# Optimization experiments

Measured on AMD Instinct MI355X. Metric: run time of the kernel, lower is better.

## Reference

```python
import jax, jax.numpy as jnp
import numpy as np
import math

N_HEADS = 16
D_HEAD = 128
D_ROPE = 32
SPLIT = D_HEAD - D_ROPE  # 96
LATENT = 512
D_MODEL = 2048
B, T = 2, 2048


def _rotary_emb(num_tokens, d_rope):
    inv_freq = 1.0 / (10000.0 ** (jnp.arange(0, d_rope, 2, dtype=jnp.float32) / d_rope))
    t = jnp.arange(num_tokens, dtype=jnp.float32)
    freqs = jnp.einsum('t,f->tf', t, inv_freq)          # [T, d_rope/2]
    return jnp.concatenate([freqs, freqs], axis=-1)      # [T, d_rope]


def _apply_rotary(x, cos, sin):
    # x: [B,T,H,d_rope]; cos/sin: [1,T,1,d_rope]
    half = x.shape[-1] // 2
    x1, x2 = x[..., :half], x[..., half:]
    rot = jnp.concatenate([-x2, x1], axis=-1)
    return x * cos + rot * sin


def setup_inputs() -> dict:
    key = jax.random.key(0)
    ks = jax.random.split(key, 20)
    s = 0.02
    def w(k, i, o):
        return jax.random.normal(k, (i, o), dtype=jnp.float32) * s
    inp = {
        'input': jax.random.normal(ks[0], (B, T, D_MODEL), dtype=jnp.float32),
        'batch_size': B,
        'num_tokens': T,
        'Wdkv_w': w(ks[1], D_MODEL, LATENT), 'Wdkv_b': jnp.zeros((LATENT,), jnp.float32),
        'Wdq_w':  w(ks[2], D_MODEL, LATENT), 'Wdq_b':  jnp.zeros((LATENT,), jnp.float32),
        'Wuk_w':  w(ks[3], LATENT, N_HEADS * SPLIT),  'Wuk_b': jnp.zeros((N_HEADS * SPLIT,), jnp.float32),
        'Wuv_w':  w(ks[4], LATENT, N_HEADS * D_HEAD), 'Wuv_b': jnp.zeros((N_HEADS * D_HEAD,), jnp.float32),
        'Wuq_w':  w(ks[5], LATENT, N_HEADS * SPLIT),  'Wuq_b': jnp.zeros((N_HEADS * SPLIT,), jnp.float32),
        'Wqr_w':  w(ks[6], LATENT, N_HEADS * D_ROPE), 'Wqr_b': jnp.zeros((N_HEADS * D_ROPE,), jnp.float32),
        'Wkr_w':  w(ks[7], D_MODEL, N_HEADS * D_ROPE), 'Wkr_b': jnp.zeros((N_HEADS * D_ROPE,), jnp.float32),
        'Wo_w':   w(ks[8], N_HEADS * D_HEAD, D_MODEL), 'Wo_b': jnp.zeros((D_MODEL,), jnp.float32),
    }
    return inp


def reference(input, batch_size, num_tokens,
              Wdkv_w, Wdkv_b, Wdq_w, Wdq_b, Wuk_w, Wuk_b, Wuv_w, Wuv_b,
              Wuq_w, Wuq_b, Wqr_w, Wqr_b, Wkr_w, Wkr_b, Wo_w, Wo_b):
    lin = lambda x, w, b: x @ w + b
    bsz, T_ = batch_size, num_tokens

    c_kv = lin(input, Wdkv_w, Wdkv_b)                                   # [B,T,latent]
    k_base = lin(c_kv, Wuk_w, Wuk_b).reshape(bsz, T_, N_HEADS, SPLIT)
    v = lin(c_kv, Wuv_w, Wuv_b).reshape(bsz, T_, N_HEADS, D_HEAD)

    c_q = lin(input, Wdq_w, Wdq_b)
    q_base = lin(c_q, Wuq_w, Wuq_b).reshape(bsz, T_, N_HEADS, SPLIT)
    q_rot = lin(c_q, Wqr_w, Wqr_b).reshape(bsz, T_, N_HEADS, D_ROPE)

    emb = _rotary_emb(T_, D_ROPE)                                        # [T,d_rope]
    cos = jnp.cos(emb)[None, :, None, :]
    sin = jnp.sin(emb)[None, :, None, :]
    q_rot = _apply_rotary(q_rot, cos, sin)
    k_rot = _apply_rotary(lin(input, Wkr_w, Wkr_b).reshape(bsz, T_, N_HEADS, D_ROPE), cos, sin)

    q = jnp.concatenate([q_base, q_rot], axis=-1)                        # [B,T,H,d_head]
    k = jnp.concatenate([k_base, k_rot], axis=-1)

    scores = jnp.einsum('bqhd,bkhd->bhqk', q, k) / math.sqrt(D_HEAD)
    attn = jax.nn.softmax(scores, axis=-1)
    out = jnp.einsum('bhqk,bkhd->bqhd', attn, v)
    out = lin(out.reshape(bsz, T_, N_HEADS * D_HEAD), Wo_w, Wo_b)
    return out, c_kv, k_rot
```

## Files before the change

kernel.cpp:

```cpp
#include <hip/hip_runtime.h>

typedef __bf16 bf16x8 __attribute__((ext_vector_type(8)));
typedef float f32x4 __attribute__((ext_vector_type(4)));
typedef float f32x16 __attribute__((ext_vector_type(16)));

#define NROWS 4096
#define DM 2048
#define LAT 512
#define NH 16
#define DH 128

__device__ __forceinline__ unsigned short f2bf(float f) {
    union { float f; unsigned u; } v; v.f = f;
    unsigned r = v.u + 0x7fffu + ((v.u >> 16) & 1u);
    return (unsigned short)(r >> 16);
}
__device__ __forceinline__ void gload16(const void* g, void* l) {
    __builtin_amdgcn_global_load_lds((const __attribute__((address_space(1))) unsigned int*)g,
                                     (__attribute__((address_space(3))) unsigned int*)l, 16, 0, 0);
}
__device__ __forceinline__ unsigned cvtpk_bf16(float lo, float hi) {
    unsigned r;
    asm("v_cvt_pk_bf16_f32 %0, %1, %2" : "=v"(r) : "v"(lo), "v"(hi));
    return r;
}
__device__ __forceinline__ void pl32swap(unsigned& a, unsigned& b) {
    asm("v_permlane32_swap_b32 %0, %1" : "+v"(a), "+v"(b));
}
__device__ __forceinline__ float exp2a(float x) {
    float r;
    asm("v_exp_f32 %0, %1" : "=v"(r) : "v"(x));
    return r;
}

struct PrepParams {
    const float* tsrc[8]; unsigned short* tdst[8];
    int tK[8]; int tN[8]; int tstart[8];
    const float* input; unsigned short* xbf;
    float* cs; float* sn;
    const float* bsrc[8]; float* bdst[8]; int blen[8];
};

#define PREP_T_END   9984
#define PREP_X_END   18176
#define PREP_R_END   18304
#define PREP_B_END   18340

__global__ __launch_bounds__(256) void prep_kernel(PrepParams P) {
    const int bid = blockIdx.x, tid = threadIdx.x;
    if (bid < PREP_T_END) {
        int j = 0;
        #pragma unroll
        for (int i = 1; i < 8; ++i) if (bid >= P.tstart[i]) j = i;
        const int local = bid - P.tstart[j];
        const float* W = P.tsrc[j];
        unsigned short* Wt = P.tdst[j];
        const int K = P.tK[j], N = P.tN[j];
        const int nbx = N >> 5;
        const int nb = (local % nbx) * 32, kb = (local / nbx) * 32;
        __shared__ float tile[32][33];
        const int tx = tid & 31, ty = tid >> 5;
        #pragma unroll
        for (int i = 0; i < 32; i += 8)
            tile[ty + i][tx] = W[(size_t)(kb + ty + i) * N + nb + tx];
        __syncthreads();
        #pragma unroll
        for (int i = 0; i < 32; i += 8)
            Wt[(size_t)(nb + ty + i) * K + kb + tx] = f2bf(tile[tx][ty + i]);
    } else if (bid < PREP_X_END) {
        const int i = ((bid - PREP_T_END) * 256 + tid) * 4;
        float4 v = *(const float4*)(P.input + i);
        unsigned short* y = P.xbf + i;
        y[0] = f2bf(v.x); y[1] = f2bf(v.y); y[2] = f2bf(v.z); y[3] = f2bf(v.w);
    } else if (bid < PREP_R_END) {
        const int idx = (bid - PREP_X_END) * 256 + tid;
        const int i = idx & 15, t = idx >> 4;
        float inv = powf(10000.0f, -(float)i / 16.0f);
        float a = (float)t * inv;
        P.cs[idx] = cosf(a);
        P.sn[idx] = sinf(a);
    } else {
        const int gid = (bid - PREP_R_END) * 256 + tid;
        int off = 0;
        #pragma unroll
        for (int i = 0; i < 8; ++i) {
            if (gid >= off && gid < off + P.blen[i])
                P.bdst[i][gid - off] = P.bsrc[i][gid - off];
            off += P.blen[i];
        }
    }
}

__global__ __launch_bounds__(256) void gemm_fused_kernel(const unsigned short* __restrict__ A,
                                                         const unsigned short* __restrict__ Bt,
                                                         const float* __restrict__ biascat,
                                                         int K, int which,
                                                         float* __restrict__ outF,
                                                         unsigned short* __restrict__ outB0,
                                                         unsigned short* __restrict__ outB1,
                                                         unsigned short* __restrict__ outB0k,
                                                         float* __restrict__ outRope,
                                                         const float* __restrict__ cs,
                                                         const float* __restrict__ sn) {
    __shared__ __align__(16) unsigned short SM[2][8192];
    const int tid = threadIdx.x;
    const int mb = blockIdx.x * 128;
    const int by = blockIdx.y, nb = by * 128;
    const int w = tid >> 6, lane = tid & 63;
    const int wr = (w >> 1) * 64, wc = (w & 1) * 64;
    const int l15 = lane & 15, l4 = lane >> 4;
    const int srow = lane >> 2, sko = (lane & 3) * 8;

    f32x4 acc[4][4] = {};

    auto STAGE = [&](int buf, int k0) {
        #pragma unroll
        for (int c = 0; c < 16; c += 4) {
            int cc = c + w;
            if (cc < 8)
                gload16(A + (size_t)(mb + cc * 16 + srow) * K + k0 + sko, SM[buf] + cc * 512);
            else
                gload16(Bt + (size_t)(nb + (cc - 8) * 16 + srow) * K + k0 + sko, SM[buf] + 4096 + (cc - 8) * 512);
        }
    };

    const int nk = K >> 5;
    STAGE(0, 0);
    for (int kt = 0; kt < nk; ++kt) {
        const int buf = kt & 1;
        if (kt + 1 < nk) {
            STAGE(buf ^ 1, (kt + 1) << 5);
            asm volatile("s_waitcnt vmcnt(4)" ::: "memory");
        } else {
            asm volatile("s_waitcnt vmcnt(0)" ::: "memory");
        }
        __builtin_amdgcn_sched_barrier(0);
        __builtin_amdgcn_s_barrier();
        __builtin_amdgcn_sched_barrier(0);

        const unsigned short* As = SM[buf];
        const unsigned short* Bs = SM[buf] + 4096;
        bf16x8 af[4], bfr[4];
        #pragma unroll
        for (int mi = 0; mi < 4; ++mi)
            af[mi] = *(const bf16x8*)(As + (wr + mi * 16 + l15) * 32 + l4 * 8);
        #pragma unroll
        for (int ni = 0; ni < 4; ++ni)
            bfr[ni] = *(const bf16x8*)(Bs + (wc + ni * 16 + l15) * 32 + l4 * 8);
        #pragma unroll
        for (int mi = 0; mi < 4; ++mi)
            #pragma unroll
            for (int ni = 0; ni < 4; ++ni)
                acc[mi][ni] = __builtin_amdgcn_mfma_f32_16x16x32_bf16(af[mi], bfr[ni], acc[mi][ni], 0, 0, 0);
        __builtin_amdgcn_s_barrier();
    }

    if (which == 1 && by >= 12) {
        unsigned short* BT = &SM[0][0];
        const int c2b = nb - 1536;
        #pragma unroll
        for (int half = 0; half < 2; ++half) {
            __syncthreads();
            if ((wr >> 6) == half) {
                #pragma unroll
                for (int mi = 0; mi < 4; ++mi)
                    #pragma unroll
                    for (int ni = 0; ni < 4; ++ni) {
                        const int col = wc + ni * 16 + l15;
                        const float bv = biascat[nb + col];
                        ushort4 pv;
                        pv.x = f2bf(acc[mi][ni][0] + bv);
                        pv.y = f2bf(acc[mi][ni][1] + bv);
                        pv.z = f2bf(acc[mi][ni][2] + bv);
                        pv.w = f2bf(acc[mi][ni][3] + bv);
                        *(ushort4*)(BT + col * 72 + mi * 16 + l4 * 4) = pv;
                    }
            }
            __syncthreads();
            const int c = tid >> 1;
            #pragma unroll
            for (int j = 0; j < 4; ++j) {
                const int seg = (tid & 1) * 4 + j;
                uint4 val = *(const uint4*)(BT + c * 72 + seg * 8);
                *(uint4*)(outB1 + (size_t)(c2b + c) * 4096 + mb + half * 64 + seg * 8) = val;
            }
        }
        return;
    }

    #pragma unroll
    for (int mi = 0; mi < 4; ++mi) {
        const int row0 = mb + wr + mi * 16 + l4 * 4;
        #pragma unroll
        for (int ni = 0; ni < 4; ++ni) {
            const int colg = nb + wc + ni * 16 + l15;
            const float bv = biascat[colg];
            float v[4];
            #pragma unroll
            for (int r = 0; r < 4; ++r) v[r] = acc[mi][ni][r] + bv;

            if (which == 0) {
                if (by < 4) {
                    #pragma unroll
                    for (int r = 0; r < 4; ++r) {
                        outF[(size_t)(row0 + r) * 512 + colg] = v[r];
                        outB0[(size_t)(row0 + r) * 512 + colg] = f2bf(v[r]);
                    }
                } else if (by < 8) {
                    const int c2 = colg - 512;
                    #pragma unroll
                    for (int r = 0; r < 4; ++r)
                        outB1[(size_t)(row0 + r) * 512 + c2] = f2bf(v[r]);
                } else {
                    const int cloc = colg - 1024, i2 = cloc & 31, h2 = cloc >> 5;
                    const float pbv = biascat[colg ^ 16];
                    const bool lo = (ni & 1) == 0;
                    #pragma unroll
                    for (int r = 0; r < 4; ++r) {
                        float vp = acc[mi][ni ^ 1][r] + pbv;
                        int t = (row0 + r) & 2047;
                        float cc_ = cs[t * 16 + (i2 & 15)], ss_ = sn[t * 16 + (i2 & 15)];
                        float o = lo ? (v[r] * cc_ - vp * ss_) : (v[r] * cc_ + vp * ss_);
                        outRope[(size_t)(row0 + r) * 512 + cloc] = o;
                        outB0k[(size_t)(row0 + r) * 2048 + h2 * 128 + 96 + i2] = f2bf(o);
                    }
                }
            } else if (which == 1) {
                const int ocol = (colg / 96) * 128 + colg % 96;
                #pragma unroll
                for (int r = 0; r < 4; ++r)
                    outB0[(size_t)(row0 + r) * 2048 + ocol] = f2bf(v[r]);
            } else if (which == 2) {
                if (by < 12) {
                    const int ocol = (colg / 96) * 128 + colg % 96;
                    #pragma unroll
                    for (int r = 0; r < 4; ++r)
                        outB0[(size_t)(row0 + r) * 2048 + ocol] = f2bf(v[r]);
                } else {
                    const int cloc = colg - 1536, i2 = cloc & 31, h2 = cloc >> 5;
                    const float pbv = biascat[colg ^ 16];
                    const bool lo = (ni & 1) == 0;
                    #pragma unroll
                    for (int r = 0; r < 4; ++r) {
                        float vp = acc[mi][ni ^ 1][r] + pbv;
                        int t = (row0 + r) & 2047;
                        float cc_ = cs[t * 16 + (i2 & 15)], ss_ = sn[t * 16 + (i2 & 15)];
                        float o = lo ? (v[r] * cc_ - vp * ss_) : (v[r] * cc_ + vp * ss_);
                        outB0[(size_t)(row0 + r) * 2048 + h2 * 128 + 96 + i2] = f2bf(o);
                    }
                }
            } else {
                #pragma unroll
                for (int r = 0; r < 4; ++r)
                    outF[(size_t)(row0 + r) * 2048 + colg] = v[r];
            }
        }
    }
}

__global__ __launch_bounds__(256, 2) void attn_kernel(const unsigned short* __restrict__ Q,
                                                      const unsigned short* __restrict__ Kb,
                                                      const unsigned short* __restrict__ Vtg,
                                                      unsigned short* __restrict__ O) {
    __shared__ __align__(16) unsigned short Ks[2][64 * 128];
    __shared__ __align__(16) unsigned short Vs[2][128 * 64];

    const int tid = threadIdx.x, w = tid >> 6, lane = tid & 63;
    const int l31 = lane & 31, hi = lane >> 5;
    const int bid = blockIdx.x;
    const int logical = (bid & 7) * 64 + (bid >> 3);
    const int bh = logical >> 4, b = bh >> 4, h = bh & 15;
    const int qt = (logical & 15) * 128 + w * 32;
    const int qrow = qt + l31;
    const float sl2e = 0.08838834764831845f * 1.4426950408889634f;

    bf16x8 qf[8];
    const unsigned short* qptr = Q + (size_t)(b * 2048 + qrow) * 2048 + h * 128 + hi * 8;
    #pragma unroll
    for (int s = 0; s < 8; ++s) qf[s] = *(const bf16x8*)(qptr + s * 16);

    f32x16 acc[4] = {};
    float m_run = -1e30f, l_run = 0.0f;

    const int kl15 = lane >> 4, kd0 = lane & 15;
    const int vr = lane >> 3, vk = lane & 7;

    auto STAGE = [&](int buf, int kt) {
        #pragma unroll
        for (int i = 0; i < 4; ++i) {
            int c = w * 4 + i;
            int key = c * 4 + kl15;
            int d0 = (kd0 * 8) ^ ((key & 7) << 3);
            gload16(Kb + (size_t)(b * 2048 + kt + key) * 2048 + h * 128 + d0, &Ks[buf][c * 512]);
            int dv = c * 8 + vr;
            int k0 = (vk * 8) ^ ((dv & 7) << 3);
            gload16(Vtg + (size_t)(h * 128 + dv) * 4096 + b * 2048 + kt + k0, &Vs[buf][c * 512]);
        }
    };

    STAGE(0, 0);

    for (int t = 0; t < 32; ++t) {
        const int buf = t & 1;
        if (t < 31) {
            STAGE(buf ^ 1, (t + 1) * 64);
            asm volatile("s_waitcnt vmcnt(8)" ::: "memory");
        } else {
            asm volatile("s_waitcnt vmcnt(0)" ::: "memory");
        }
        __builtin_amdgcn_sched_barrier(0);
        __builtin_amdgcn_s_barrier();
        __builtin_amdgcn_sched_barrier(0);

        #pragma unroll
        for (int g = 0; g < 2; ++g) {
            const int key = g * 32 + l31;
            const unsigned short* kbase = &Ks[buf][key * 128];
            const int ksw = (key & 7) << 3;
            f32x16 sc = {};
            __builtin_amdgcn_s_setprio(1);
            #pragma unroll
            for (int s = 0; s < 8; ++s) {
                bf16x8 kf = *(const bf16x8*)(kbase + ((s * 16 + hi * 8) ^ ksw));
                sc = __builtin_amdgcn_mfma_f32_32x32x16_bf16(kf, qf[s], sc, 0, 0, 0);
            }
            __builtin_amdgcn_s_setprio(0);

            float pm = sc[0];
            #pragma unroll
            for (int i = 1; i < 16; ++i) pm = fmaxf(pm, sc[i]);
            pm = fmaxf(pm, __shfl_xor(pm, 32, 64));

            if (__any(pm > m_run + 90.51f)) {
                float mn = fmaxf(m_run, pm);
                float f = exp2a((m_run - mn) * sl2e);
                m_run = mn;
                l_run *= f;
                #pragma unroll
                for (int dg = 0; dg < 4; ++dg)
                    #pragma unroll
                    for (int i = 0; i < 16; ++i) acc[dg][i] *= f;
            }
            const float mexp2 = m_run * sl2e;

            float rs = 0.0f;
            #pragma unroll
            for (int s2 = 0; s2 < 2; ++s2) {
                float e[8];
                #pragma unroll
                for (int j = 0; j < 8; ++j) {
                    e[j] = exp2a(fmaf(sc[s2 * 8 + j], sl2e, -mexp2));
                    rs += e[j];
                }
                unsigned X0 = cvtpk_bf16(e[0], e[1]), X1 = cvtpk_bf16(e[2], e[3]);
                unsigned Y0 = cvtpk_bf16(e[4], e[5]), Y1 = cvtpk_bf16(e[6], e[7]);
                pl32swap(X0, Y0);
                pl32swap(X1, Y1);
                union { unsigned u[4]; bf16x8 v; } pf;
                pf.u[0] = X0; pf.u[1] = X1; pf.u[2] = Y0; pf.u[3] = Y1;

                const int kofs = g * 32 + s2 * 16 + hi * 8;
                __builtin_amdgcn_s_setprio(1);
                #pragma unroll
                for (int dg = 0; dg < 4; ++dg) {
                    const int d = dg * 32 + l31;
                    bf16x8 vf = *(const bf16x8*)(&Vs[buf][d * 64 + (kofs ^ ((d & 7) << 3))]);
                    acc[dg] = __builtin_amdgcn_mfma_f32_32x32x16_bf16(vf, pf.v, acc[dg], 0, 0, 0);
                }
                __builtin_amdgcn_s_setprio(0);
            }
            rs += __shfl_xor(rs, 32, 64);
            l_run += rs;
        }
        __builtin_amdgcn_s_barrier();
    }

    const float inv = 1.0f / l_run;
    unsigned short* obase = O + (size_t)(b * 2048 + qrow) * 2048 + h * 128;
    #pragma unroll
    for (int dg = 0; dg < 4; ++dg)
        #pragma unroll
        for (int k = 0; k < 4; ++k) {
            ushort4 pv;
            pv.x = f2bf(acc[dg][4 * k + 0] * inv);
            pv.y = f2bf(acc[dg][4 * k + 1] * inv);
            pv.z = f2bf(acc[dg][4 * k + 2] * inv);
            pv.w = f2bf(acc[dg][4 * k + 3] * inv);
            *(ushort4*)(obase + dg * 32 + k * 8 + hi * 4) = pv;
        }
}

extern "C" void kernel_launch(void* const* d_in, const int* in_sizes, int n_in,
                              void* d_out, int out_size, void* d_ws, size_t ws_size,
                              hipStream_t stream) {
    (void)in_sizes; (void)n_in; (void)out_size; (void)ws_size;

    const float* input  = (const float*)d_in[0];
    const float* Wdkv_w = (const float*)d_in[3];
    const float* Wdkv_b = (const float*)d_in[4];
    const float* Wdq_w  = (const float*)d_in[5];
    const float* Wdq_b  = (const float*)d_in[6];
    const float* Wuk_w  = (const float*)d_in[7];
    const float* Wuk_b  = (const float*)d_in[8];
    const float* Wuv_w  = (const float*)d_in[9];
    const float* Wuv_b  = (const float*)d_in[10];
    const float* Wuq_w  = (const float*)d_in[11];
    const float* Wuq_b  = (const float*)d_in[12];
    const float* Wqr_w  = (const float*)d_in[13];
    const float* Wqr_b  = (const float*)d_in[14];
    const float* Wkr_w  = (const float*)d_in[15];
    const float* Wkr_b  = (const float*)d_in[16];
    const float* Wo_w   = (const float*)d_in[17];
    const float* Wo_b   = (const float*)d_in[18];

    float* out_main = (float*)d_out;
    float* out_ckv  = out_main + (size_t)NROWS * DM;
    float* out_krot = out_ckv + (size_t)NROWS * LAT;

    char* p = (char*)d_ws;
    auto alloc = [&](size_t bytes) { char* r = p; p += (bytes + 255) & ~(size_t)255; return r; };
    unsigned short* x_bf  = (unsigned short*)alloc((size_t)NROWS * DM * 2);
    unsigned short* w1_t  = (unsigned short*)alloc((size_t)1536 * DM * 2);
    unsigned short* w2_t  = (unsigned short*)alloc((size_t)3584 * LAT * 2);
    unsigned short* w3_t  = (unsigned short*)alloc((size_t)2048 * LAT * 2);
    unsigned short* w4_t  = (unsigned short*)alloc((size_t)DM * DM * 2);
    unsigned short* ckv_bf = (unsigned short*)alloc((size_t)NROWS * LAT * 2);
    unsigned short* cq_bf  = (unsigned short*)alloc((size_t)NROWS * LAT * 2);
    unsigned short* q_bf   = (unsigned short*)alloc((size_t)NROWS * DM * 2);
    unsigned short* k_bf   = (unsigned short*)alloc((size_t)NROWS * DM * 2);
    unsigned short* vt_g   = (unsigned short*)alloc((size_t)DM * NROWS * 2);
    unsigned short* ao_bf  = (unsigned short*)alloc((size_t)NROWS * DM * 2);
    float* cos_t = (float*)alloc((size_t)2048 * 16 * 4);
    float* sin_t = (float*)alloc((size_t)2048 * 16 * 4);
    float* bc1 = (float*)alloc(1536 * 4);
    float* bc2 = (float*)alloc(3584 * 4);
    float* bc3 = (float*)alloc(2048 * 4);
    float* bc4 = (float*)alloc(2048 * 4);

    PrepParams P;
    const float* tsrc[8] = {Wdkv_w, Wdq_w, Wkr_w, Wuk_w, Wuv_w, Wuq_w, Wqr_w, Wo_w};
    unsigned short* tdst[8] = {w1_t, w1_t + 512 * 2048, w1_t + 1024 * 2048,
                               w2_t, w2_t + 1536 * 512, w3_t, w3_t + 1536 * 512, w4_t};
    int tK[8] = {2048, 2048, 2048, 512, 512, 512, 512, 2048};
    int tN[8] = {512, 512, 512, 1536, 2048, 1536, 512, 2048};
    int tstart[8] = {0, 1024, 2048, 3072, 3840, 4864, 5632, 5888};
    const float* bsrc[8] = {Wdkv_b, Wdq_b, Wkr_b, Wuk_b, Wuv_b, Wuq_b, Wqr_b, Wo_b};
    float* bdst[8] = {bc1, bc1 + 512, bc1 + 1024, bc2, bc2 + 1536, bc3, bc3 + 1536, bc4};
    int blen[8] = {512, 512, 512, 1536, 2048, 1536, 512, 2048};
    for (int i = 0; i < 8; ++i) {
        P.tsrc[i] = tsrc[i]; P.tdst[i] = tdst[i]; P.tK[i] = tK[i]; P.tN[i] = tN[i];
        P.tstart[i] = tstart[i]; P.bsrc[i] = bsrc[i]; P.bdst[i] = bdst[i]; P.blen[i] = blen[i];
    }
    P.input = input; P.xbf = x_bf; P.cs = cos_t; P.sn = sin_t;
    prep_kernel<<<PREP_B_END, 256, 0, stream>>>(P);

    gemm_fused_kernel<<<dim3(32, 12), 256, 0, stream>>>(x_bf, w1_t, bc1, 2048, 0,
                                                        out_ckv, ckv_bf, cq_bf, k_bf, out_krot, cos_t, sin_t);
    gemm_fused_kernel<<<dim3(32, 28), 256, 0, stream>>>(ckv_bf, w2_t, bc2, 512, 1,
                                                        nullptr, k_bf, vt_g, nullptr, nullptr, nullptr, nullptr);
    gemm_fused_kernel<<<dim3(32, 16), 256, 0, stream>>>(cq_bf, w3_t, bc3, 512, 2,
                                                        nullptr, q_bf, nullptr, nullptr, nullptr, cos_t, sin_t);

    attn_kernel<<<512, 256, 0, stream>>>(q_bf, k_bf, vt_g, ao_bf);

    gemm_fused_kernel<<<dim3(32, 16), 256, 0, stream>>>(ao_bf, w4_t, bc4, 2048, 3,
                                                        out_main, nullptr, nullptr, nullptr, nullptr, nullptr, nullptr);
}
```

Before: 239.0 us.

## Merge up-projection GEMMs, retile first GEMM to 192 cols, swizzle blocks, restructure attention

Combines the K/V up-projection and Q up-projection GEMMs into a single launch over a concatenated weight buffer. A second A pointer selects the Q latent for the upper column blocks. The first GEMM is templated to a 192-wide N tile so it runs as 256 blocks, roughly one wave on the device, and block indices are remapped with an XCD-style swizzle. In attention, the two key-group score MFMA chains are interleaved and the max and sum reductions become trees to shorten dependency chains. These changes bring more register pressure and more complex epilogue column routing.

```diff
diff --git a/kernel.cpp b/kernel.cpp
--- a/kernel.cpp
+++ b/kernel.cpp
@@ -91,7 +91,9 @@
     }
 }
 
+template<int BN>
 __global__ __launch_bounds__(256) void gemm_fused_kernel(const unsigned short* __restrict__ A,
+                                                         const unsigned short* __restrict__ A2,
                                                          const unsigned short* __restrict__ Bt,
                                                          const float* __restrict__ biascat,
                                                          int K, int which,
@@ -102,23 +104,31 @@
                                                          float* __restrict__ outRope,
                                                          const float* __restrict__ cs,
                                                          const float* __restrict__ sn) {
-    __shared__ __align__(16) unsigned short SM[2][8192];
+    constexpr int NF = BN / 32;
+    constexpr int NCH = 8 + BN / 16;
+    constexpr int BUFSZ = 4096 + BN * 32;
+    __shared__ __align__(16) unsigned short SM[2][BUFSZ];
     const int tid = threadIdx.x;
-    const int mb = blockIdx.x * 128;
-    const int by = blockIdx.y, nb = by * 128;
+    const int cpx = gridDim.x >> 3;
+    const int logical = (blockIdx.x & 7) * cpx + (blockIdx.x >> 3);
+    const int mb = (logical & 31) * 128;
+    const int by = logical >> 5;
+    const int nb = by * BN;
     const int w = tid >> 6, lane = tid & 63;
-    const int wr = (w >> 1) * 64, wc = (w & 1) * 64;
+    const int wr = (w >> 1) * 64, wc = (w & 1) * (BN / 2);
     const int l15 = lane & 15, l4 = lane >> 4;
     const int srow = lane >> 2, sko = (lane & 3) * 8;
 
-    f32x4 acc[4][4] = {};
+    const unsigned short* Ause = (which == 1 && by >= 28) ? A2 : A;
+
+    f32x4 acc[4][NF] = {};
 
     auto STAGE = [&](int buf, int k0) {
         #pragma unroll
-        for (int c = 0; c < 16; c += 4) {
+        for (int c = 0; c < NCH; c += 4) {
             int cc = c + w;
             if (cc < 8)
-                gload16(A + (size_t)(mb + cc * 16 + srow) * K + k0 + sko, SM[buf] + cc * 512);
+                gload16(Ause + (size_t)(mb + cc * 16 + srow) * K + k0 + sko, SM[buf] + cc * 512);
             else
                 gload16(Bt + (size_t)(nb + (cc - 8) * 16 + srow) * K + k0 + sko, SM[buf] + 4096 + (cc - 8) * 512);
         }
@@ -130,7 +140,8 @@
         const int buf = kt & 1;
         if (kt + 1 < nk) {
             STAGE(buf ^ 1, (kt + 1) << 5);
-            asm volatile("s_waitcnt vmcnt(4)" ::: "memory");
+            if constexpr (NCH == 16) asm volatile("s_waitcnt vmcnt(4)" ::: "memory");
+            else                     asm volatile("s_waitcnt vmcnt(5)" ::: "memory");
         } else {
             asm volatile("s_waitcnt vmcnt(0)" ::: "memory");
         }
@@ -140,22 +151,22 @@
 
         const unsigned short* As = SM[buf];
         const unsigned short* Bs = SM[buf] + 4096;
-        bf16x8 af[4], bfr[4];
+        bf16x8 af[4], bfr[NF];
         #pragma unroll
         for (int mi = 0; mi < 4; ++mi)
             af[mi] = *(const bf16x8*)(As + (wr + mi * 16 + l15) * 32 + l4 * 8);
         #pragma unroll
-        for (int ni = 0; ni < 4; ++ni)
+        for (int ni = 0; ni < NF; ++ni)
             bfr[ni] = *(const bf16x8*)(Bs + (wc + ni * 16 + l15) * 32 + l4 * 8);
         #pragma unroll
         for (int mi = 0; mi < 4; ++mi)
             #pragma unroll
-            for (int ni = 0; ni < 4; ++ni)
+            for (int ni = 0; ni < NF; ++ni)
                 acc[mi][ni] = __builtin_amdgcn_mfma_f32_16x16x32_bf16(af[mi], bfr[ni], acc[mi][ni], 0, 0, 0);
         __builtin_amdgcn_s_barrier();
     }
 
-    if (which == 1 && by >= 12) {
+    if (which == 1 && by >= 12 && by < 28) {
         unsigned short* BT = &SM[0][0];
         const int c2b = nb - 1536;
         #pragma unroll
@@ -165,7 +176,7 @@
                 #pragma unroll
                 for (int mi = 0; mi < 4; ++mi)
                     #pragma unroll
-                    for (int ni = 0; ni < 4; ++ni) {
+                    for (int ni = 0; ni < NF; ++ni) {
                         const int col = wc + ni * 16 + l15;
                         const float bv = biascat[nb + col];
                         ushort4 pv;
@@ -192,7 +203,7 @@
     for (int mi = 0; mi < 4; ++mi) {
         const int row0 = mb + wr + mi * 16 + l4 * 4;
         #pragma unroll
-        for (int ni = 0; ni < 4; ++ni) {
+        for (int ni = 0; ni < NF; ++ni) {
             const int colg = nb + wc + ni * 16 + l15;
             const float bv = biascat[colg];
             float v[4];
@@ -200,13 +211,13 @@
             for (int r = 0; r < 4; ++r) v[r] = acc[mi][ni][r] + bv;
 
             if (which == 0) {
-                if (by < 4) {
+                if (colg < 512) {
                     #pragma unroll
                     for (int r = 0; r < 4; ++r) {
                         outF[(size_t)(row0 + r) * 512 + colg] = v[r];
                         outB0[(size_t)(row0 + r) * 512 + colg] = f2bf(v[r]);
                     }
-                } else if (by < 8) {
+                } else if (colg < 1024) {
                     const int c2 = colg - 512;
                     #pragma unroll
                     for (int r = 0; r < 4; ++r)
@@ -226,18 +237,19 @@
                     }
                 }
             } else if (which == 1) {
-                const int ocol = (colg / 96) * 128 + colg % 96;
-                #pragma unroll
-                for (int r = 0; r < 4; ++r)
-                    outB0[(size_t)(row0 + r) * 2048 + ocol] = f2bf(v[r]);
-            } else if (which == 2) {
                 if (by < 12) {
                     const int ocol = (colg / 96) * 128 + colg % 96;
                     #pragma unroll
                     for (int r = 0; r < 4; ++r)
                         outB0[(size_t)(row0 + r) * 2048 + ocol] = f2bf(v[r]);
+                } else if (by < 40) {
+                    const int c3 = colg - 3584;
+                    const int ocol = (c3 / 96) * 128 + c3 % 96;
+                    #pragma unroll
+                    for (int r = 0; r < 4; ++r)
+                        outB0k[(size_t)(row0 + r) * 2048 + ocol] = f2bf(v[r]);
                 } else {
-                    const int cloc = colg - 1536, i2 = cloc & 31, h2 = cloc >> 5;
+                    const int cloc = colg - 5120, i2 = cloc & 31, h2 = cloc >> 5;
                     const float pbv = biascat[colg ^ 16];
                     const bool lo = (ni & 1) == 0;
                     #pragma unroll
@@ -246,7 +258,7 @@
                         int t = (row0 + r) & 2047;
                         float cc_ = cs[t * 16 + (i2 & 15)], ss_ = sn[t * 16 + (i2 & 15)];
                         float o = lo ? (v[r] * cc_ - vp * ss_) : (v[r] * cc_ + vp * ss_);
-                        outB0[(size_t)(row0 + r) * 2048 + h2 * 128 + 96 + i2] = f2bf(o);
+                        outB0k[(size_t)(row0 + r) * 2048 + h2 * 128 + 96 + i2] = f2bf(o);
                     }
                 }
             } else {
@@ -312,23 +324,27 @@
         __builtin_amdgcn_s_barrier();
         __builtin_amdgcn_sched_barrier(0);
 
-        #pragma unroll
-        for (int g = 0; g < 2; ++g) {
-            const int key = g * 32 + l31;
-            const unsigned short* kbase = &Ks[buf][key * 128];
-            const int ksw = (key & 7) << 3;
-            f32x16 sc = {};
-            __builtin_amdgcn_s_setprio(1);
-            #pragma unroll
-            for (int s = 0; s < 8; ++s) {
-                bf16x8 kf = *(const bf16x8*)(kbase + ((s * 16 + hi * 8) ^ ksw));
-                sc = __builtin_amdgcn_mfma_f32_32x32x16_bf16(kf, qf[s], sc, 0, 0, 0);
-            }
-            __builtin_amdgcn_s_setprio(0);
-
-            float pm = sc[0];
-            #pragma unroll
-            for (int i = 1; i < 16; ++i) pm = fmaxf(pm, sc[i]);
+        const unsigned short* kb0 = &Ks[buf][l31 * 128];
+        const int ksw = (l31 & 7) << 3;
+        f32x16 sc0 = {}, sc1 = {};
+        __builtin_amdgcn_s_setprio(1);
+        #pragma unroll
+        for (int s = 0; s < 8; ++s) {
+            const int off = (s * 16 + hi * 8) ^ ksw;
+            bf16x8 kf0 = *(const bf16x8*)(kb0 + off);
+            bf16x8 kf1 = *(const bf16x8*)(kb0 + 32 * 128 + off);
+            sc0 = __builtin_amdgcn_mfma_f32_32x32x16_bf16(kf0, qf[s], sc0, 0, 0, 0);
+            sc1 = __builtin_amdgcn_mfma_f32_32x32x16_bf16(kf1, qf[s], sc1, 0, 0, 0);
+        }
+        __builtin_amdgcn_s_setprio(0);
+
+        auto SMPV = [&](f32x16& sc, int g) {
+            float t0 = fmaxf(sc[0], sc[1]),  t1 = fmaxf(sc[2], sc[3]);
+            float t2 = fmaxf(sc[4], sc[5]),  t3 = fmaxf(sc[6], sc[7]);
+            float t4 = fmaxf(sc[8], sc[9]),  t5 = fmaxf(sc[10], sc[11]);
+            float t6 = fmaxf(sc[12], sc[13]), t7 = fmaxf(sc[14], sc[15]);
+            float pm = fmaxf(fmaxf(fmaxf(t0, t1), fmaxf(t2, t3)),
+                             fmaxf(fmaxf(t4, t5), fmaxf(t6, t7)));
             pm = fmaxf(pm, __shfl_xor(pm, 32, 64));
 
             if (__any(pm > m_run + 90.51f)) {
@@ -343,17 +359,15 @@
             }
             const float mexp2 = m_run * sl2e;
 
-            float rs = 0.0f;
+            float e[16];
+            #pragma unroll
+            for (int j = 0; j < 16; ++j)
+                e[j] = exp2a(fmaf(sc[j], sl2e, -mexp2));
+
             #pragma unroll
             for (int s2 = 0; s2 < 2; ++s2) {
-                float e[8];
-                #pragma unroll
-                for (int j = 0; j < 8; ++j) {
-                    e[j] = exp2a(fmaf(sc[s2 * 8 + j], sl2e, -mexp2));
-                    rs += e[j];
-                }
-                unsigned X0 = cvtpk_bf16(e[0], e[1]), X1 = cvtpk_bf16(e[2], e[3]);
-                unsigned Y0 = cvtpk_bf16(e[4], e[5]), Y1 = cvtpk_bf16(e[6], e[7]);
+                unsigned X0 = cvtpk_bf16(e[s2 * 8 + 0], e[s2 * 8 + 1]), X1 = cvtpk_bf16(e[s2 * 8 + 2], e[s2 * 8 + 3]);
+                unsigned Y0 = cvtpk_bf16(e[s2 * 8 + 4], e[s2 * 8 + 5]), Y1 = cvtpk_bf16(e[s2 * 8 + 6], e[s2 * 8 + 7]);
                 pl32swap(X0, Y0);
                 pl32swap(X1, Y1);
                 union { unsigned u[4]; bf16x8 v; } pf;
@@ -369,9 +383,15 @@
                 }
                 __builtin_amdgcn_s_setprio(0);
             }
+            float a0 = e[0] + e[1], a1 = e[2] + e[3], a2 = e[4] + e[5], a3 = e[6] + e[7];
+            float a4 = e[8] + e[9], a5 = e[10] + e[11], a6 = e[12] + e[13], a7 = e[14] + e[15];
+            float rs = ((a0 + a1) + (a2 + a3)) + ((a4 + a5) + (a6 + a7));
             rs += __shfl_xor(rs, 32, 64);
             l_run += rs;
-        }
+        };
+        SMPV(sc0, 0);
+        SMPV(sc1, 1);
+
         __builtin_amdgcn_s_barrier();
     }
 
@@ -421,8 +441,7 @@
     auto alloc = [&](size_t bytes) { char* r = p; p += (bytes + 255) & ~(size_t)255; return r; };
     unsigned short* x_bf  = (unsigned short*)alloc((size_t)NROWS * DM * 2);
     unsigned short* w1_t  = (unsigned short*)alloc((size_t)1536 * DM * 2);
-    unsigned short* w2_t  = (unsigned short*)alloc((size_t)3584 * LAT * 2);
-    unsigned short* w3_t  = (unsigned short*)alloc((size_t)2048 * LAT * 2);
+    unsigned short* w23_t = (unsigned short*)alloc((size_t)5632 * LAT * 2);
     unsigned short* w4_t  = (unsigned short*)alloc((size_t)DM * DM * 2);
     unsigned short* ckv_bf = (unsigned short*)alloc((size_t)NROWS * LAT * 2);
     unsigned short* cq_bf  = (unsigned short*)alloc((size_t)NROWS * LAT * 2);
@@ -432,20 +451,19 @@
     unsigned short* ao_bf  = (unsigned short*)alloc((size_t)NROWS * DM * 2);
     float* cos_t = (float*)alloc((size_t)2048 * 16 * 4);
     float* sin_t = (float*)alloc((size_t)2048 * 16 * 4);
-    float* bc1 = (float*)alloc(1536 * 4);
-    float* bc2 = (float*)alloc(3584 * 4);
-    float* bc3 = (float*)alloc(2048 * 4);
-    float* bc4 = (float*)alloc(2048 * 4);
+    float* bc1  = (float*)alloc(1536 * 4);
+    float* bc23 = (float*)alloc(5632 * 4);
+    float* bc4  = (float*)alloc(2048 * 4);
 
     PrepParams P;
     const float* tsrc[8] = {Wdkv_w, Wdq_w, Wkr_w, Wuk_w, Wuv_w, Wuq_w, Wqr_w, Wo_w};
     unsigned short* tdst[8] = {w1_t, w1_t + 512 * 2048, w1_t + 1024 * 2048,
-                               w2_t, w2_t + 1536 * 512, w3_t, w3_t + 1536 * 512, w4_t};
+                               w23_t, w23_t + 1536 * 512, w23_t + 3584 * 512, w23_t + 5120 * 512, w4_t};
     int tK[8] = {2048, 2048, 2048, 512, 512, 512, 512, 2048};
     int tN[8] = {512, 512, 512, 1536, 2048, 1536, 512, 2048};
     int tstart[8] = {0, 1024, 2048, 3072, 3840, 4864, 5632, 5888};
     const float* bsrc[8] = {Wdkv_b, Wdq_b, Wkr_b, Wuk_b, Wuv_b, Wuq_b, Wqr_b, Wo_b};
-    float* bdst[8] = {bc1, bc1 + 512, bc1 + 1024, bc2, bc2 + 1536, bc3, bc3 + 1536, bc4};
+    float* bdst[8] = {bc1, bc1 + 512, bc1 + 1024, bc23, bc23 + 1536, bc23 + 3584, bc23 + 5120, bc4};
     int blen[8] = {512, 512, 512, 1536, 2048, 1536, 512, 2048};
     for (int i = 0; i < 8; ++i) {
         P.tsrc[i] = tsrc[i]; P.tdst[i] = tdst[i]; P.tK[i] = tK[i]; P.tN[i] = tN[i];
@@ -454,15 +472,13 @@
     P.input = input; P.xbf = x_bf; P.cs = cos_t; P.sn = sin_t;
     prep_kernel<<<PREP_B_END, 256, 0, stream>>>(P);
 
-    gemm_fused_kernel<<<dim3(32, 12), 256, 0, stream>>>(x_bf, w1_t, bc1, 2048, 0,
-                                                        out_ckv, ckv_bf, cq_bf, k_bf, out_krot, cos_t, sin_t);
-    gemm_fused_kernel<<<dim3(32, 28), 256, 0, stream>>>(ckv_bf, w2_t, bc2, 512, 1,
-                                                        nullptr, k_bf, vt_g, nullptr, nullptr, nullptr, nullptr);
-    gemm_fused_kernel<<<dim3(32, 16), 256, 0, stream>>>(cq_bf, w3_t, bc3, 512, 2,
-                                                        nullptr, q_bf, nullptr, nullptr, nullptr, cos_t, sin_t);
+    gemm_fused_kernel<192><<<256, 256, 0, stream>>>(x_bf, nullptr, w1_t, bc1, 2048, 0,
+                                                    out_ckv, ckv_bf, cq_bf, k_bf, out_krot, cos_t, sin_t);
+    gemm_fused_kernel<128><<<1408, 256, 0, stream>>>(ckv_bf, cq_bf, w23_t, bc23, 512, 1,
+                                                     nullptr, k_bf, vt_g, q_bf, nullptr, cos_t, sin_t);
 
     attn_kernel<<<512, 256, 0, stream>>>(q_bf, k_bf, vt_g, ao_bf);
 
-    gemm_fused_kernel<<<dim3(32, 16), 256, 0, stream>>>(ao_bf, w4_t, bc4, 2048, 3,
-                                                        out_main, nullptr, nullptr, nullptr, nullptr, nullptr, nullptr);
-}
+    gemm_fused_kernel<128><<<512, 256, 0, stream>>>(ao_bf, nullptr, w4_t, bc4, 2048, 3,
+                                                    out_main, nullptr, nullptr, nullptr, nullptr, nullptr, nullptr);
+}
```

After: 258.1 us. 8.0% more time.
